# Kernel optimization log

Hardware: AMD Instinct MI355X
Metric: run time of the kernel (lower is better)

## Reference

```python
import jax, jax.numpy as jnp
import numpy as np

M, K = 4096, 4096
ORDER = 12  # ceil(log2(max(M,K)))
BATCH, SEQ = 4, 2048


def _hilbert_d_grid(order, m, k):
    """Vectorized xy->d Hilbert-curve index for an m x k grid (numpy, int)."""
    n = 1 << order
    ii, jj = np.meshgrid(np.arange(m, dtype=np.int64), np.arange(k, dtype=np.int64), indexing='ij')
    x, y = jj.copy(), ii.copy()
    d = np.zeros_like(x)
    s = n >> 1
    while s > 0:
        rx = ((x & s) > 0).astype(np.int64)
        ry = ((y & s) > 0).astype(np.int64)
        d += s * s * ((3 * rx) ^ ry)
        # rotate quadrant
        swap = ry == 0
        flip = swap & (rx == 1)
        xf = np.where(flip, s - 1 - x, x)
        yf = np.where(flip, s - 1 - y, y)
        x = np.where(swap, yf, xf)
        y = np.where(swap, xf, yf)
        s >>= 1
    return d.astype(np.int32)


def setup_inputs() -> dict:
    key = jax.random.key(0)
    k1, = jax.random.split(key, 1)
    x = jax.random.normal(k1, (BATCH, SEQ, K), dtype=jnp.float32)
    # dna init per __init__: [4.0,1.0,1.0,0.5,0.5,0.5] with dna[0] += (seed%100)/10 for seed=42
    dna = jnp.array([8.2, 1.0, 1.0, 0.5, 0.5, 0.5], dtype=jnp.float32)
    bias = jnp.zeros((M,), dtype=jnp.float32)
    hilbert_d = jnp.asarray(_hilbert_d_grid(ORDER, M, K))  # [M, K] int32
    return {"x": x, "dna": dna, "bias": bias, "hilbert_d": hilbert_d}


def reference(x, dna, bias, hilbert_d):
    # dna is detached in the torch forward (weights built from numpy copy)
    p = jax.lax.stop_gradient(dna)
    m_p, a, b, n1, n2, n3 = p[0], p[1], p[2], p[3], p[4], p[5]
    total = jnp.float32((1 << ORDER) * (1 << ORDER))
    theta = hilbert_d.astype(jnp.float32) * (2.0 * jnp.pi / total)  # [M,K]
    ang = m_p * theta * 0.25
    base = jnp.abs(jnp.cos(ang) / a) ** n2 + jnp.abs(jnp.sin(ang) / b) ** n3
    r = base ** (-1.0 / n1)  # Gielis superformula radius, [M,K]
    w = (r - r.mean()) / (jnp.std(r, ddof=1) + 1e-9)  # torch .std() is unbiased
    scale = jnp.float32(1.0 / np.sqrt(K))
    return jnp.einsum('bsk,mk->bsm', x, w) * scale + bias
```

## Files before the change

### kernel.cpp

```cpp
#include <hip/hip_runtime.h>

#define M_DIM 4096
#define K_DIM 4096
#define NR_DIM 8192
#define TOTAL_ELEMS (M_DIM * K_DIM)

typedef unsigned short u16;
typedef unsigned int u32;
typedef __bf16 bf16x8 __attribute__((ext_vector_type(8)));
typedef float f32x4 __attribute__((ext_vector_type(4)));
typedef u16 u16x8 __attribute__((ext_vector_type(8)));

__device__ __forceinline__ u16 f2b(float f) {
    u32 v;
    __builtin_memcpy(&v, &f, sizeof(v));
    v += 0x7FFFu + ((v >> 16) & 1u);
    return (u16)(v >> 16);
}

__device__ __forceinline__ void abs_sincos(float ang, float* s, float* c) {
    float q = rintf(ang * 0.636619772f);
    float r1 = fmaf(q, -1.57079637e+00f, ang);
    float r = fmaf(q, 4.37113883e-08f, r1);
    float r2 = r * r;
    float ts = fmaf(r2, -1.9840874e-04f, 8.3333310e-03f);
    ts = fmaf(r2, ts, -1.6666667e-01f);
    float sp = fmaf(r * r2, ts, r);
    float tc = fmaf(r2, -1.3888378e-03f, 4.1666638e-02f);
    tc = fmaf(r2, tc, -5.0e-01f);
    float cp = fmaf(r2, tc, 1.0f);
    bool sw = (((int)q) & 1) != 0;
    *s = sw ? cp : sp;
    *c = sw ? sp : cp;
}

__device__ __forceinline__ float compute_r_fast(int d, float c_ang) {
    float s, c;
    abs_sincos((float)d * c_ang, &s, &c);
    float base = __builtin_amdgcn_sqrtf(fabsf(c)) + __builtin_amdgcn_sqrtf(fabsf(s));
    return __builtin_amdgcn_rcpf(base * base);
}

__device__ __noinline__ float compute_r_gen(int d, float c_ang, float inv_a,
                                            float inv_b, float n2, float n3, float e) {
    float s, c;
    abs_sincos((float)d * c_ang, &s, &c);
    float ca = fabsf(c) * fabsf(inv_a);
    float sb = fabsf(s) * fabsf(inv_b);
    float t1 = (n2 == 0.5f) ? sqrtf(ca) : ((n2 == 1.0f) ? ca : powf(ca, n2));
    float t2 = (n3 == 0.5f) ? sqrtf(sb) : ((n3 == 1.0f) ? sb : powf(sb, n3));
    float base = t1 + t2;
    if (e == -2.0f) { float ib = __builtin_amdgcn_rcpf(base); return ib * ib; }
    if (e == -1.0f) return __builtin_amdgcn_rcpf(base);
    return powf(base, e);
}

__device__ __forceinline__ bool dna_is_fast(const float* p) {
    return (p[1] == 1.0f) & (p[2] == 1.0f) & (p[3] == 0.5f) &
           (p[4] == 0.5f) & (p[5] == 0.5f);
}

__global__ void __launch_bounds__(256) reduce_kernel(const float* __restrict__ dna,
                                                     double* __restrict__ sums) {
    float p[6];
#pragma unroll
    for (int i = 0; i < 6; i++) p[i] = dna[i];
    float c_ang = (float)((double)p[0] * 6.283185307179586 / 67108864.0);

    double s = 0.0, s2 = 0.0;
    int idx = blockIdx.x * blockDim.x + threadIdx.x;
    int stride = gridDim.x * blockDim.x;
    if (dna_is_fast(p)) {
        for (int d = idx; d < TOTAL_ELEMS; d += stride) {
            float r = compute_r_fast(d, c_ang);
            s += (double)r;
            s2 += (double)r * (double)r;
        }
    } else {
        float inv_a = 1.0f / p[1], inv_b = 1.0f / p[2], e = -1.0f / p[3];
        for (int d = idx; d < TOTAL_ELEMS; d += stride) {
            float r = compute_r_gen(d, c_ang, inv_a, inv_b, p[4], p[5], e);
            s += (double)r;
            s2 += (double)r * (double)r;
        }
    }
#pragma unroll
    for (int off = 32; off > 0; off >>= 1) {
        s += __shfl_down(s, off);
        s2 += __shfl_down(s2, off);
    }
    __shared__ double ls[4], ls2[4];
    int lane = threadIdx.x & 63, w = threadIdx.x >> 6;
    if (lane == 0) { ls[w] = s; ls2[w] = s2; }
    __syncthreads();
    if (threadIdx.x == 0) {
        atomicAdd(&sums[0], ls[0] + ls[1] + ls[2] + ls[3]);
        atomicAdd(&sums[1], ls2[0] + ls2[1] + ls2[2] + ls2[3]);
    }
}

__global__ void __launch_bounds__(256) build_w_kernel(const int* __restrict__ hd,
                                                      const float* __restrict__ dna,
                                                      const double* __restrict__ sums,
                                                      u16* __restrict__ W) {
    float p[6];
#pragma unroll
    for (int i = 0; i < 6; i++) p[i] = dna[i];
    float c_ang = (float)((double)p[0] * 6.283185307179586 / 67108864.0);

    const double cnt = (double)TOTAL_ELEMS;
    double sum = sums[0], sumsq = sums[1];
    float meanf = (float)(sum / cnt);
    float stdf = (float)sqrt((sumsq - sum * sum / cnt) / (cnt - 1.0));
    float sc = 0.015625f / (stdf + 1e-9f);

    int idx = blockIdx.x * blockDim.x + threadIdx.x;
    int stride = gridDim.x * blockDim.x;
    if (dna_is_fast(p)) {
        for (int i = idx * 4; i < TOTAL_ELEMS; i += stride * 4) {
            int4 d4 = *(const int4*)(hd + i);
            ushort4 o;
            o.x = f2b((compute_r_fast(d4.x, c_ang) - meanf) * sc);
            o.y = f2b((compute_r_fast(d4.y, c_ang) - meanf) * sc);
            o.z = f2b((compute_r_fast(d4.z, c_ang) - meanf) * sc);
            o.w = f2b((compute_r_fast(d4.w, c_ang) - meanf) * sc);
            *(ushort4*)(W + i) = o;
        }
    } else {
        float inv_a = 1.0f / p[1], inv_b = 1.0f / p[2], e = -1.0f / p[3];
        for (int i = idx * 4; i < TOTAL_ELEMS; i += stride * 4) {
            int4 d4 = *(const int4*)(hd + i);
            ushort4 o;
            o.x = f2b((compute_r_gen(d4.x, c_ang, inv_a, inv_b, p[4], p[5], e) - meanf) * sc);
            o.y = f2b((compute_r_gen(d4.y, c_ang, inv_a, inv_b, p[4], p[5], e) - meanf) * sc);
            o.z = f2b((compute_r_gen(d4.z, c_ang, inv_a, inv_b, p[4], p[5], e) - meanf) * sc);
            o.w = f2b((compute_r_gen(d4.w, c_ang, inv_a, inv_b, p[4], p[5], e) - meanf) * sc);
            *(ushort4*)(W + i) = o;
        }
    }
}

__global__ void __launch_bounds__(256) convert_x_kernel(const float* __restrict__ x,
                                                        u16* __restrict__ xb) {
    int i = (blockIdx.x * blockDim.x + threadIdx.x) * 8;
    const float4* xv = (const float4*)(x + i);
    float4 a = xv[0], b = xv[1];
    u16x8 o;
    o[0] = f2b(a.x); o[1] = f2b(a.y); o[2] = f2b(a.z); o[3] = f2b(a.w);
    o[4] = f2b(b.x); o[5] = f2b(b.y); o[6] = f2b(b.z); o[7] = f2b(b.w);
    *(u16x8*)(xb + i) = o;
}

#define BM 256
#define BN 256
#define BK 64

__device__ __forceinline__ void gld_lds16(const u16* g, u16* l) {
    __builtin_amdgcn_global_load_lds(
        (const __attribute__((address_space(1))) void*)g,
        (__attribute__((address_space(3))) void*)l,
        16, 0, 0);
}

#define FENCE asm volatile("" ::: "memory")
#define WAIT_VM6 asm volatile("s_waitcnt vmcnt(6)" ::: "memory")

#define ISSUE_AF(dst, bufv, ks, h)                                            \
    _Pragma("unroll") for (int m = 0; m < 4; ++m) {                           \
        int row = wr * 128 + ((h) * 4 + m) * 16 + lrow;                       \
        dst[m] = *(const bf16x8*)(&sA[bufv][ks][row * 32 + oA]);              \
    }

#define ISSUE_BF(dst, bufv, ks)                                               \
    _Pragma("unroll") for (int n = 0; n < 4; ++n) {                           \
        int row = wc * 64 + n * 16 + lrow;                                    \
        dst[n] = *(const bf16x8*)(&sB[bufv][ks][row * 32 + oA]);              \
    }

#define MFMA_HALF(h, afb, bfb)                                                \
    __builtin_amdgcn_s_setprio(1);                                            \
    _Pragma("unroll") for (int m = 0; m < 4; ++m)                             \
        _Pragma("unroll") for (int n = 0; n < 4; ++n)                         \
            acc[(h) * 4 + m][n] = __builtin_amdgcn_mfma_f32_16x16x32_bf16(    \
                afb[m], bfb[n], acc[(h) * 4 + m][n], 0, 0, 0);                \
    __builtin_amdgcn_s_setprio(0)

__global__ void __launch_bounds__(512, 2) gemm_kernel(const u16* __restrict__ A,
                                                      const u16* __restrict__ B,
                                                      const float* __restrict__ bias,
                                                      float* __restrict__ C) {
    __shared__ __align__(16) u16 sA[2][2][BM * 32];
    __shared__ __align__(16) u16 sB[2][2][BN * 32];

    const int tid = threadIdx.x;
    const int lane = tid & 63;
    const int wave = tid >> 6;
    const int wr = wave >> 2;
    const int wc = wave & 3;
    const int lrow = lane & 15;
    const int lq = lane >> 4;
    const int oA = ((lq ^ ((lrow >> 1) & 3)) << 3);

    const int flat = blockIdx.y * 16 + blockIdx.x;
    const int swz = (flat & 7) * 64 + (flat >> 3);
    const int bx = swz & 15;
    const int by = swz >> 4;
    const int i0 = by * BM;
    const int j0 = bx * BN;

    const int srow0 = tid >> 2;
    const int olog = (tid & 3) ^ ((srow0 >> 1) & 3);
    const int aoff0 = (i0 + srow0) * K_DIM + olog * 8;
    const int aoff1 = aoff0 + 128 * K_DIM;
    const int boff0 = (j0 + srow0) * K_DIM + olog * 8;
    const int boff1 = boff0 + 128 * K_DIM;
    const int lds_l0 = tid * 8;
    const int lds_l1 = (tid + 512) * 8;

    auto stage = [&](const u16* base, int off0, int off1, u16* slot, int kb) {
        gld_lds16(base + off0 + kb, slot + lds_l0);
        gld_lds16(base + off1 + kb, slot + lds_l1);
    };

    const f32x4 vzero = {0.f, 0.f, 0.f, 0.f};
    f32x4 acc[8][4];
#pragma unroll
    for (int a = 0; a < 8; a++)
#pragma unroll
        for (int b = 0; b < 4; b++) acc[a][b] = vzero;

    stage(A, aoff0, aoff1, sA[0][0], 0);
    stage(B, boff0, boff1, sB[0][0], 0);
    stage(A, aoff0, aoff1, sA[0][1], 32);
    stage(B, boff0, boff1, sB[0][1], 32);
    stage(A, aoff0, aoff1, sA[1][0], 64);
    stage(B, boff0, boff1, sB[1][0], 64);
    WAIT_VM6;
    FENCE;
    __builtin_amdgcn_s_barrier();

    bf16x8 af_a[4], af_b[4], bfr[4];
    ISSUE_AF(af_a, 0, 0, 0);
    FENCE;

    for (int kt = 0; kt < K_DIM / BK; ++kt) {
        const int bufv = kt & 1;
        const int kb1 = (kt + 1 < 64 ? kt + 1 : 63) * 64 + 32;
        const int kb2 = (kt + 2 < 64 ? kt + 2 : 63) * 64;

        ISSUE_BF(bfr, bufv, 0);
        ISSUE_AF(af_b, bufv, 0, 1);
        stage(A, aoff0, aoff1, sA[bufv ^ 1][1], kb1);
        FENCE;
        __builtin_amdgcn_s_barrier();
        MFMA_HALF(0, af_a, bfr);
        FENCE;
        __builtin_amdgcn_s_barrier();

        ISSUE_AF(af_a, bufv, 1, 0);
        stage(B, boff0, boff1, sB[bufv ^ 1][1], kb1);
        FENCE;
        __builtin_amdgcn_s_barrier();
        MFMA_HALF(1, af_b, bfr);
        WAIT_VM6;
        FENCE;
        __builtin_amdgcn_s_barrier();

        ISSUE_BF(bfr, bufv, 1);
        ISSUE_AF(af_b, bufv, 1, 1);
        stage(A, aoff0, aoff1, sA[bufv][0], kb2);
        FENCE;
        __builtin_amdgcn_s_barrier();
        MFMA_HALF(0, af_a, bfr);
        FENCE;
        __builtin_amdgcn_s_barrier();

        ISSUE_AF(af_a, bufv ^ 1, 0, 0);
        stage(B, boff0, boff1, sB[bufv][0], kb2);
        FENCE;
        __builtin_amdgcn_s_barrier();
        MFMA_HALF(1, af_b, bfr);
        WAIT_VM6;
        FENCE;
        __builtin_amdgcn_s_barrier();
    }

#pragma unroll
    for (int ni = 0; ni < 4; ++ni) {
        long j = j0 + wc * 64 + ni * 16 + lrow;
        float bv = bias[j];
#pragma unroll
        for (int mi = 0; mi < 8; ++mi) {
            long ib = i0 + wr * 128 + mi * 16 + lq * 4;
#pragma unroll
            for (int r = 0; r < 4; ++r) {
                C[(ib + r) * M_DIM + j] = acc[mi][ni][r] + bv;
            }
        }
    }
}

extern "C" void kernel_launch(void* const* d_in, const int* in_sizes, int n_in,
                              void* d_out, int out_size, void* d_ws, size_t ws_size,
                              hipStream_t stream) {
    const float* x = (const float*)d_in[0];
    const float* dna = (const float*)d_in[1];
    const float* bias = (const float*)d_in[2];
    const int* hd = (const int*)d_in[3];
    float* out = (float*)d_out;

    double* sums = (double*)d_ws;
    u16* W = (u16*)((char*)d_ws + 256);
    u16* Xb = (u16*)((char*)d_ws + 256 + (size_t)TOTAL_ELEMS * 2);

    hipMemsetAsync(d_ws, 0, 256, stream);
    reduce_kernel<<<dim3(1024), dim3(256), 0, stream>>>(dna, sums);
    build_w_kernel<<<dim3(2048), dim3(256), 0, stream>>>(hd, dna, sums, W);
    convert_x_kernel<<<dim3((NR_DIM * K_DIM) / (256 * 8)), dim3(256), 0, stream>>>(x, Xb);
    gemm_kernel<<<dim3(M_DIM / BN, NR_DIM / BM), dim3(512), 0, stream>>>(Xb, W, bias, out);
}
```

Before: 610.7 us.

## Halve barriers per k-step and double-buffer B fragments in GEMM main loop

Restructures the GEMM inner loop so each quarter-step issues its LDS fragment loads and the next global-to-LDS stage, then runs MFMAs behind a scheduling barrier. This removes one of the two workgroup barriers per phase. B fragments are now double-buffered (bfA/bfB) so they can be prefetched a phase earlier, and the vmcnt waits are re-placed. This adds register pressure and relies on correct vmcnt accounting for LDS buffer reuse, which risks races if the counts are off.

After: 574.9 us. -5.9%, faster.

```diff
diff --git a/kernel.cpp b/kernel.cpp
--- a/kernel.cpp
+++ b/kernel.cpp
@@ -164,14 +164,16 @@
 
 #define FENCE asm volatile("" ::: "memory")
 #define WAIT_VM6 asm volatile("s_waitcnt vmcnt(6)" ::: "memory")
-
-#define ISSUE_AF(dst, bufv, ks, h)                                            \
+#define WAIT_VM4 asm volatile("s_waitcnt vmcnt(4)" ::: "memory")
+#define SB0 __builtin_amdgcn_sched_barrier(0)
+
+#define ISSUE_A(dst, bufv, ks, h)                                             \
     _Pragma("unroll") for (int m = 0; m < 4; ++m) {                           \
         int row = wr * 128 + ((h) * 4 + m) * 16 + lrow;                       \
         dst[m] = *(const bf16x8*)(&sA[bufv][ks][row * 32 + oA]);              \
     }
 
-#define ISSUE_BF(dst, bufv, ks)                                               \
+#define ISSUE_B(dst, bufv, ks)                                                \
     _Pragma("unroll") for (int n = 0; n < 4; ++n) {                           \
         int row = wc * 64 + n * 16 + lrow;                                    \
         dst[n] = *(const bf16x8*)(&sB[bufv][ks][row * 32 + oA]);              \
@@ -235,12 +237,13 @@
     stage(B, boff0, boff1, sB[0][1], 32);
     stage(A, aoff0, aoff1, sA[1][0], 64);
     stage(B, boff0, boff1, sB[1][0], 64);
-    WAIT_VM6;
+    WAIT_VM4;
     FENCE;
     __builtin_amdgcn_s_barrier();
 
-    bf16x8 af_a[4], af_b[4], bfr[4];
-    ISSUE_AF(af_a, 0, 0, 0);
+    bf16x8 afA[4], afB[4], bfA[4], bfB[4];
+    ISSUE_A(afA, 0, 0, 0);
+    ISSUE_B(bfA, 0, 0);
     FENCE;
 
     for (int kt = 0; kt < K_DIM / BK; ++kt) {
@@ -248,39 +251,35 @@
         const int kb1 = (kt + 1 < 64 ? kt + 1 : 63) * 64 + 32;
         const int kb2 = (kt + 2 < 64 ? kt + 2 : 63) * 64;
 
-        ISSUE_BF(bfr, bufv, 0);
-        ISSUE_AF(af_b, bufv, 0, 1);
+        ISSUE_A(afB, bufv, 0, 1);
         stage(A, aoff0, aoff1, sA[bufv ^ 1][1], kb1);
-        FENCE;
-        __builtin_amdgcn_s_barrier();
-        MFMA_HALF(0, af_a, bfr);
-        FENCE;
-        __builtin_amdgcn_s_barrier();
-
-        ISSUE_AF(af_a, bufv, 1, 0);
-        stage(B, boff0, boff1, sB[bufv ^ 1][1], kb1);
-        FENCE;
-        __builtin_amdgcn_s_barrier();
-        MFMA_HALF(1, af_b, bfr);
+        SB0;
+        MFMA_HALF(0, afA, bfA);
         WAIT_VM6;
         FENCE;
         __builtin_amdgcn_s_barrier();
 
-        ISSUE_BF(bfr, bufv, 1);
-        ISSUE_AF(af_b, bufv, 1, 1);
-        stage(A, aoff0, aoff1, sA[bufv][0], kb2);
+        ISSUE_A(afA, bufv, 1, 0);
+        ISSUE_B(bfB, bufv, 1);
+        stage(B, boff0, boff1, sB[bufv ^ 1][1], kb1);
+        SB0;
+        MFMA_HALF(1, afB, bfA);
         FENCE;
         __builtin_amdgcn_s_barrier();
-        MFMA_HALF(0, af_a, bfr);
+
+        ISSUE_A(afB, bufv, 1, 1);
+        stage(A, aoff0, aoff1, sA[bufv][0], kb2);
+        SB0;
+        MFMA_HALF(0, afA, bfB);
+        WAIT_VM6;
         FENCE;
         __builtin_amdgcn_s_barrier();
 
-        ISSUE_AF(af_a, bufv ^ 1, 0, 0);
+        ISSUE_A(afA, bufv ^ 1, 0, 0);
+        ISSUE_B(bfA, bufv ^ 1, 0);
         stage(B, boff0, boff1, sB[bufv][0], kb2);
-        FENCE;
-        __builtin_amdgcn_s_barrier();
-        MFMA_HALF(1, af_b, bfr);
-        WAIT_VM6;
+        SB0;
+        MFMA_HALF(1, afB, bfB);
         FENCE;
         __builtin_amdgcn_s_barrier();
     }
```
